# Kernel tuning notes

Hardware: AMD Instinct MI355X
Metric: run time of the kernel (lower is better)

## Reference

```python
import jax, jax.numpy as jnp
import numpy as np

NH, NKV, HD = 16, 8, 128  # heads, kv heads, head dim
N_REP = NH // NKV
EPS = 1e-06
K_MASK = float(jnp.finfo(jnp.bfloat16).min)
SCALE = HD ** -0.5


def _rms_norm(x, w):
    xf = x.astype(jnp.float32)
    rms = jnp.sqrt(jnp.mean(xf * xf, axis=-1, keepdims=True) + EPS)
    return (xf / rms * w).astype(x.dtype)


def _rotate_half(x):
    x1, x2 = jnp.split(x, 2, axis=-1)
    return jnp.concatenate([-x2, x1], axis=-1)


def setup_inputs() -> dict:
    key = jax.random.key(0)
    ks = jax.random.split(key, 5)
    B, S, H = 1, 2048, 2048
    hidden_states = jax.random.normal(ks[0], (B, S, H), jnp.float32)
    # real RoPE tables (duplicated-half layout), theta = 5e6
    pos = jnp.arange(S, dtype=jnp.float32)
    inv_freq = 1.0 / (5_000_000.0 ** (jnp.arange(0, HD, 2, dtype=jnp.float32) / HD))
    ang = pos[:, None] * inv_freq[None, :]            # (S, HD/2)
    emb = jnp.concatenate([ang, ang], axis=-1)[None]  # (1, S, HD)
    cos, sin = jnp.cos(emb), jnp.sin(emb)
    attention_mask = jnp.tril(jnp.ones((S, S), bool))[None, None]  # causal (1,1,S,S)
    sc = 0.02
    wq = jax.random.normal(ks[1], (H, NH * HD), jnp.float32) * sc
    wk = jax.random.normal(ks[2], (H, NKV * HD), jnp.float32) * sc
    wv = jax.random.normal(ks[3], (H, NKV * HD), jnp.float32) * sc
    wo = jax.random.normal(ks[4], (NH * HD, H), jnp.float32) * sc
    q_norm_w = jnp.ones((HD,), jnp.float32)
    k_norm_w = jnp.ones((HD,), jnp.float32)
    return {"hidden_states": hidden_states, "cos": cos, "sin": sin,
            "attention_mask": attention_mask, "wq": wq, "wk": wk, "wv": wv,
            "wo": wo, "q_norm_w": q_norm_w, "k_norm_w": k_norm_w}


def reference(hidden_states, cos, sin, attention_mask, wq, wk, wv, wo, q_norm_w, k_norm_w):
    B, S, H = hidden_states.shape
    q = (hidden_states @ wq).reshape(B, S, NH, HD)
    k = (hidden_states @ wk).reshape(B, S, NKV, HD)
    v = (hidden_states @ wv).reshape(B, S, NKV, HD)
    q = _rms_norm(q, q_norm_w)
    k = _rms_norm(k, k_norm_w)
    c = cos[:, :, None, :]
    s = sin[:, :, None, :]
    q = q * c + _rotate_half(q) * s
    k = k * c + _rotate_half(k) * s
    # GQA: group q heads by kv head; same math as jnp.repeat + matmul
    qg = q.reshape(B, S, NKV, N_REP, HD)
    scores = jnp.einsum('bqgrd,bkgd->bgrqk', qg, k) * SCALE  # (B,NKV,N_REP,S,S)
    scores = jnp.where(attention_mask[:, :, None], scores, K_MASK)
    attn = jax.nn.softmax(scores.astype(jnp.float32), axis=-1).astype(q.dtype)
    out = jnp.einsum('bgrqk,bkgd->bqgrd', attn, v)            # (B,S,NKV,N_REP,HD)
    out = out.reshape(B, S, NH * HD)
    return out @ wo
```

## Files before the change

kernel.cpp:

```cpp
#include <hip/hip_runtime.h>
#include <hip/hip_bf16.h>
#include <stdint.h>

typedef _Float16 half8 __attribute__((ext_vector_type(8)));
typedef _Float16 half4 __attribute__((ext_vector_type(4)));
typedef float f32x4 __attribute__((ext_vector_type(4)));

#define MFMA16(A, B, C) __builtin_amdgcn_mfma_f32_16x16x32_f16(A, B, C, 0, 0, 0)

static constexpr int Sdim = 2048;
static constexpr int NH = 16;
static constexpr int NKV = 8;
static constexpr int HD = 128;
static constexpr float ATT_SCALE = 0.08838834764831845f;
static constexpr float S0 = 4.0f;

__device__ __forceinline__ void async_copy16(const _Float16* g, _Float16* l) {
  auto gp = reinterpret_cast<const __attribute__((address_space(1))) uint32_t*>(
      reinterpret_cast<uintptr_t>(g));
  auto lp = reinterpret_cast<__attribute__((address_space(3))) uint32_t*>(
      reinterpret_cast<uintptr_t>(l));
  __builtin_amdgcn_global_load_lds(gp, lp, 16, 0, 0);
}

__global__ __launch_bounds__(256) void xconv(const float* __restrict__ X,
                                             _Float16* __restrict__ Xh) {
  int i = (blockIdx.x * 256 + threadIdx.x) * 4;
  float4 v = *(const float4*)(X + i);
  half4 h = {(_Float16)v.x, (_Float16)v.y, (_Float16)v.z, (_Float16)v.w};
  *(half4*)(Xh + i) = h;
}

__global__ __launch_bounds__(256) void wtrans_all(const float* __restrict__ wq,
                                                  const float* __restrict__ wk,
                                                  const float* __restrict__ wv,
                                                  const float* __restrict__ wo,
                                                  _Float16* __restrict__ wqT,
                                                  _Float16* __restrict__ wkT,
                                                  _Float16* __restrict__ wvT,
                                                  _Float16* __restrict__ woT) {
  const float* W;
  _Float16* WT;
  int N;
  switch (blockIdx.z) {
    case 0: W = wq; WT = wqT; N = 2048; break;
    case 1: W = wk; WT = wkT; N = 1024; break;
    case 2: W = wv; WT = wvT; N = 1024; break;
    default: W = wo; WT = woT; N = 2048; break;
  }
  if ((int)blockIdx.x * 64 >= N) return;
  const int K = 2048;
  __shared__ __align__(16) float tile[64][68];
  int n0 = blockIdx.x * 64, k0 = blockIdx.y * 64;
  int t = threadIdx.x;
  int c = (t & 15) * 4;
  int rb = t >> 4;
  for (int p = 0; p < 4; ++p) {
    int k = p * 16 + rb;
    *(float4*)&tile[k][c] = *(const float4*)(W + (size_t)(k0 + k) * N + n0 + c);
  }
  __syncthreads();
  int n = t >> 2;
  int kc = (t & 3) * 16;
  half8 o0, o1;
  for (int i = 0; i < 8; ++i) {
    o0[i] = (_Float16)tile[kc + i][n];
    o1[i] = (_Float16)tile[kc + 8 + i][n];
  }
  _Float16* dst = WT + (size_t)(n0 + n) * K + k0 + kc;
  *(half8*)dst = o0;
  *(half8*)(dst + 8) = o1;
}

template <int NI>
__device__ __forceinline__ void stage64(const _Float16* __restrict__ src, size_t stride,
                                        int k0, _Float16* lds, int w, int lane) {
  for (int ii = 0; ii < NI; ++ii) {
    int i = w * NI + ii;
    int row = i * 8 + (lane >> 3);
    int c = (lane & 7) ^ (row & 7);
    async_copy16(src + (size_t)row * stride + k0 + c * 8, lds + i * 512);
  }
}

__device__ __forceinline__ int frag_off(int row, int ks, int quad, int col) {
  return row * 64 + (((ks << 2) | quad) ^ (col & 7)) * 8;
}

__global__ __launch_bounds__(256, 2) void gemm_qkv(const _Float16* __restrict__ Xh,
                                                   const _Float16* __restrict__ wqT,
                                                   const _Float16* __restrict__ wkT,
                                                   const _Float16* __restrict__ wvT,
                                                   const float* __restrict__ cs,
                                                   const float* __restrict__ sn,
                                                   const float* __restrict__ qw,
                                                   const float* __restrict__ kw,
                                                   _Float16* __restrict__ Qn,
                                                   _Float16* __restrict__ Kn,
                                                   _Float16* __restrict__ Vt) {
  __shared__ __align__(16) _Float16 SH[4 * 128 * 64];
  int bx = blockIdx.x, m0 = blockIdx.y * 128;
  const _Float16* BT;
  _Float16* outp;
  int n0, Nst;
  bool vt;
  if (bx < 16)      { BT = wqT; outp = Qn; n0 = bx * 128;        vt = false; Nst = 2048; }
  else if (bx < 24) { BT = wkT; outp = Kn; n0 = (bx - 16) * 128; vt = false; Nst = 1024; }
  else              { BT = wvT; outp = Vt; n0 = (bx - 24) * 128; vt = true;  Nst = 2048; }
  int t = threadIdx.x, lane = t & 63, w = t >> 6;
  int col = lane & 15, quad = lane >> 4;
  int wm = (w & 1) * 64, wn = (w >> 1) * 64;
  const _Float16* Ap = Xh + (size_t)m0 * 2048;
  const _Float16* Bp = BT + (size_t)n0 * 2048;
  f32x4 acc[4][4] = {};
  stage64<4>(Ap, 2048, 0, SH, w, lane);
  stage64<4>(Bp, 2048, 0, SH + 16384, w, lane);
#pragma unroll 1
  for (int it = 0; it < 32; ++it) {
    int c = it & 1;
    if (it + 1 < 32) {
      stage64<4>(Ap, 2048, (it + 1) * 64, SH + (c ^ 1) * 8192, w, lane);
      stage64<4>(Bp, 2048, (it + 1) * 64, SH + 16384 + (c ^ 1) * 8192, w, lane);
      asm volatile("s_waitcnt vmcnt(8)" ::: "memory");
    } else {
      asm volatile("s_waitcnt vmcnt(0)" ::: "memory");
    }
    __builtin_amdgcn_sched_barrier(0);
    __builtin_amdgcn_s_barrier();
    __builtin_amdgcn_sched_barrier(0);
    const _Float16* Asc = SH + c * 8192;
    const _Float16* Bsc = SH + 16384 + c * 8192;
    half8 af[4][2], bf[4][2];
    for (int i = 0; i < 4; ++i)
      for (int ks = 0; ks < 2; ++ks) {
        af[i][ks] = *(const half8*)(Asc + frag_off(wm + i * 16 + col, ks, quad, col));
        bf[i][ks] = *(const half8*)(Bsc + frag_off(wn + i * 16 + col, ks, quad, col));
      }
    __builtin_amdgcn_s_setprio(1);
    if (!vt) {
      for (int ks = 0; ks < 2; ++ks)
        for (int i = 0; i < 4; ++i)
          for (int j = 0; j < 4; ++j)
            acc[i][j] = MFMA16(bf[j][ks], af[i][ks], acc[i][j]);
    } else {
      for (int ks = 0; ks < 2; ++ks)
        for (int i = 0; i < 4; ++i)
          for (int j = 0; j < 4; ++j)
            acc[i][j] = MFMA16(af[i][ks], bf[j][ks], acc[i][j]);
    }
    __builtin_amdgcn_s_setprio(0);
    __builtin_amdgcn_sched_barrier(0);
    __builtin_amdgcn_s_barrier();
    __builtin_amdgcn_sched_barrier(0);
  }
  if (!vt) {
    __syncthreads();
    for (int i = 0; i < 4; ++i)
      for (int j = 0; j < 4; ++j) {
        int m = wm + i * 16 + col;
        int d = wn + j * 16 + quad * 4;
        half4 hv = {(_Float16)acc[i][j][0], (_Float16)acc[i][j][1],
                    (_Float16)acc[i][j][2], (_Float16)acc[i][j][3]};
        *(half4*)(SH + m * 132 + d) = hv;
      }
    __syncthreads();
    const float* nw = (bx < 16) ? qw : kw;
    float scale = (bx < 16) ? ATT_SCALE : 1.0f;
    float w0 = nw[lane], w1 = nw[lane + 64];
#pragma unroll 1
    for (int it2 = 0; it2 < 32; it2 += 4) {
      float x0[4], x1[4], c0[4], c1[4], sv0[4], sv1[4];
#pragma unroll
      for (int u = 0; u < 4; ++u) {
        int row = w * 32 + it2 + u;
        int m = m0 + row;
        c0[u] = cs[m * HD + lane];
        c1[u] = cs[m * HD + lane + 64];
        sv0[u] = sn[m * HD + lane];
        sv1[u] = sn[m * HD + lane + 64];
        x0[u] = (float)SH[row * 132 + lane];
        x1[u] = (float)SH[row * 132 + 64 + lane];
      }
#pragma unroll
      for (int u = 0; u < 4; ++u) {
        float ss = x0[u] * x0[u] + x1[u] * x1[u];
#pragma unroll
        for (int o = 32; o > 0; o >>= 1) ss += __shfl_xor(ss, o);
        float inv = rsqrtf(ss * (1.0f / 128.0f) + 1e-6f);
        float n0v = x0[u] * inv * w0, n1v = x1[u] * inv * w1;
        int m = m0 + w * 32 + it2 + u;
        _Float16* q = outp + (size_t)m * Nst + n0;
        q[lane] = (_Float16)((n0v * c0[u] - n1v * sv0[u]) * scale);
        q[lane + 64] = (_Float16)((n1v * c1[u] + n0v * sv1[u]) * scale);
      }
    }
  } else {
    for (int i = 0; i < 4; ++i)
      for (int j = 0; j < 4; ++j) {
        int n = n0 + wn + j * 16 + col;
        int mb = m0 + wm + i * 16 + quad * 4;
        half4 hv = {(_Float16)acc[i][j][0], (_Float16)acc[i][j][1],
                    (_Float16)acc[i][j][2], (_Float16)acc[i][j][3]};
        *(half4*)(outp + (size_t)n * Sdim + mb) = hv;
      }
  }
}

__global__ __launch_bounds__(256, 2) void gemm_o(const _Float16* __restrict__ A,
                                                 const _Float16* __restrict__ BT,
                                                 float* __restrict__ C) {
  __shared__ __align__(16) _Float16 As[2][64 * 64];
  __shared__ __align__(16) _Float16 Bs[2][128 * 64];
  int m0 = blockIdx.y * 64, n0 = blockIdx.x * 128;
  int t = threadIdx.x, lane = t & 63, w = t >> 6;
  int col = lane & 15, quad = lane >> 4;
  int wm = (w & 1) * 32, wn = (w >> 1) * 64;
  const _Float16* Ap = A + (size_t)m0 * 2048;
  const _Float16* Bp = BT + (size_t)n0 * 2048;
  f32x4 acc[2][4] = {};
  stage64<2>(Ap, 2048, 0, As[0], w, lane);
  stage64<4>(Bp, 2048, 0, Bs[0], w, lane);
#pragma unroll 1
  for (int it = 0; it < 32; ++it) {
    int c = it & 1;
    if (it + 1 < 32) {
      stage64<2>(Ap, 2048, (it + 1) * 64, As[c ^ 1], w, lane);
      stage64<4>(Bp, 2048, (it + 1) * 64, Bs[c ^ 1], w, lane);
      asm volatile("s_waitcnt vmcnt(6)" ::: "memory");
    } else {
      asm volatile("s_waitcnt vmcnt(0)" ::: "memory");
    }
    __builtin_amdgcn_sched_barrier(0);
    __builtin_amdgcn_s_barrier();
    __builtin_amdgcn_sched_barrier(0);
    half8 af[2][2], bf[4][2];
    for (int ks = 0; ks < 2; ++ks) {
      for (int i = 0; i < 2; ++i)
        af[i][ks] = *(const half8*)(As[c] + frag_off(wm + i * 16 + col, ks, quad, col));
      for (int j = 0; j < 4; ++j)
        bf[j][ks] = *(const half8*)(Bs[c] + frag_off(wn + j * 16 + col, ks, quad, col));
    }
    __builtin_amdgcn_s_setprio(1);
    for (int ks = 0; ks < 2; ++ks)
      for (int i = 0; i < 2; ++i)
        for (int j = 0; j < 4; ++j)
          acc[i][j] = MFMA16(bf[j][ks], af[i][ks], acc[i][j]);
    __builtin_amdgcn_s_setprio(0);
    __builtin_amdgcn_sched_barrier(0);
    __builtin_amdgcn_s_barrier();
    __builtin_amdgcn_sched_barrier(0);
  }
  for (int i = 0; i < 2; ++i)
    for (int j = 0; j < 4; ++j) {
      int m = m0 + wm + i * 16 + col;
      int n = n0 + wn + j * 16 + quad * 4;
      *(f32x4*)(C + (size_t)m * 2048 + n) = acc[i][j];
    }
}

__device__ __forceinline__ void attn_tile(const half8* qf, f32x4* O, float& li,
                                          const _Float16* Ksb, const _Float16* Vsb,
                                          _Float16* Psw, bool domask,
                                          int col, int quad, int w) {
  f32x4 Sc[4];
  __builtin_amdgcn_s_setprio(1);
  for (int nt = 0; nt < 4; ++nt) {
    f32x4 a = {};
    for (int kc = 0; kc < 4; ++kc) {
      half8 b = *(const half8*)(Ksb + (nt * 16 + col) * 128 + ((4 * kc + quad) ^ col) * 8);
      a = MFMA16(b, qf[kc], a);
    }
    Sc[nt] = a;
  }
  __builtin_amdgcn_s_setprio(0);
  if (domask) {
    for (int nt = 0; nt < 4; ++nt)
      for (int r = 0; r < 4; ++r)
        if ((nt * 16 + quad * 4 + r) > (w * 16 + col)) Sc[nt][r] = -1e4f;
  }
  for (int nt = 0; nt < 4; ++nt) {
    half4 pk;
    for (int r = 0; r < 4; ++r) {
      float pv = __expf(Sc[nt][r] - S0);
      li += pv;
      pk[r] = (_Float16)pv;
    }
    *(half4*)(Psw + col * 64 + (((2 * nt + (quad >> 1)) ^ (col & 7)) << 3) +
              ((quad & 1) << 2)) = pk;
  }
  __builtin_amdgcn_s_setprio(1);
  for (int c2 = 0; c2 < 2; ++c2) {
    half8 ap = *(const half8*)(Psw + col * 64 + (((4 * c2 + quad) ^ (col & 7)) * 8));
    for (int nt = 0; nt < 8; ++nt) {
      half8 bv = *(const half8*)(Vsb + (nt * 16 + col) * 64 +
                                 (((4 * c2 + quad) ^ (col & 7)) * 8));
      O[nt] = MFMA16(ap, bv, O[nt]);
    }
  }
  __builtin_amdgcn_s_setprio(0);
}

__global__ __launch_bounds__(256, 2) void fattn(const _Float16* __restrict__ Qn,
                                                const _Float16* __restrict__ Kn,
                                                const _Float16* __restrict__ Vt,
                                                _Float16* __restrict__ Op01,
                                                float* __restrict__ lp) {
  __shared__ __align__(16) _Float16 Ks[2][64 * 128];
  __shared__ __align__(16) _Float16 Vs[2][128 * 64];
  __shared__ __align__(16) _Float16 Ps[4 * 1024];
  int f = blockIdx.x;
  int Wk = (f & 7) * 64 + (f >> 3);
  int xb = Wk & 15, h = (Wk >> 4) & 15, s = Wk >> 8;
  int g = h >> 1;
  int qb0 = 31 - xb, qb1 = xb;
  int t = threadIdx.x, lane = t & 63, w = t >> 6;
  int col = lane & 15, quad = lane >> 4;
  _Float16* Psw = Ps + w * 1024;
  _Float16* op = Op01 + (size_t)s * Sdim * (NH * HD);
  float* lpp = lp + (size_t)s * NH * Sdim + (size_t)h * Sdim;

  auto stageKV = [&](int b, int kt) {
    for (int ii = 0; ii < 4; ++ii) {
      int i = w * 4 + ii;
      int krow = i * 4 + (lane >> 4);
      int kc = (lane & 15) ^ (krow & 15);
      async_copy16(Kn + (size_t)(kt * 64 + krow) * (NKV * HD) + g * HD + kc * 8,
                   Ks[b] + i * 512);
      int vrow = i * 8 + (lane >> 3);
      int vc = (lane & 7) ^ (vrow & 7);
      async_copy16(Vt + (size_t)(g * HD + vrow) * Sdim + kt * 64 + vc * 8,
                   Vs[b] + i * 512);
    }
  };

  half8 qf0[4], qf1[4];
  {
    int qr0 = qb0 * 64 + w * 16 + col;
    int qr1 = qb1 * 64 + w * 16 + col;
    for (int kc = 0; kc < 4; ++kc) {
      qf0[kc] = *(const half8*)(Qn + (size_t)qr0 * (NH * HD) + h * HD + kc * 32 + quad * 8);
      qf1[kc] = *(const half8*)(Qn + (size_t)qr1 * (NH * HD) + h * HD + kc * 32 + quad * 8);
    }
  }
  f32x4 O0[8] = {}, O1[8] = {};
  float li0 = 0.0f, li1 = 0.0f;

  int nt = (qb0 - s) / 2 + 1;
  stageKV(0, s);
#pragma unroll 1
  for (int it = 0; it < nt; ++it) {
    int kt = s + it * 2;
    int c = it & 1;
    if (it + 1 < nt) {
      stageKV(c ^ 1, kt + 2);
      asm volatile("s_waitcnt vmcnt(8)" ::: "memory");
    } else {
      asm volatile("s_waitcnt vmcnt(0)" ::: "memory");
    }
    __builtin_amdgcn_sched_barrier(0);
    __builtin_amdgcn_s_barrier();
    __builtin_amdgcn_sched_barrier(0);
    const _Float16* Kb = Ks[c];
    const _Float16* Vb = Vs[c];
    if (kt <= qb1) {
      attn_tile(qf0, O0, li0, Kb, Vb, Psw, false, col, quad, w);
      attn_tile(qf1, O1, li1, Kb, Vb, Psw, kt == qb1, col, quad, w);
    } else {
      attn_tile(qf0, O0, li0, Kb, Vb, Psw, kt == qb0, col, quad, w);
    }
    __builtin_amdgcn_sched_barrier(0);
    __builtin_amdgcn_s_barrier();
    __builtin_amdgcn_sched_barrier(0);
  }

  auto finish = [&](f32x4* O, float li, int qb) {
    li += __shfl_xor(li, 16);
    li += __shfl_xor(li, 32);
    for (int ntile = 0; ntile < 8; ++ntile)
      for (int r = 0; r < 4; ++r) {
        int m = qb * 64 + w * 16 + quad * 4 + r;
        op[(size_t)m * (NH * HD) + h * HD + ntile * 16 + col] = (_Float16)O[ntile][r];
      }
    if (quad == 0) lpp[qb * 64 + w * 16 + col] = li;
  };
  finish(O0, li0, qb0);
  finish(O1, li1, qb1);
}

__global__ __launch_bounds__(256) void merge(const _Float16* __restrict__ Op01,
                                             const float* __restrict__ lp,
                                             _Float16* __restrict__ attn) {
  int m = blockIdx.x, t = threadIdx.x;
  int h = t >> 4, d0 = (t & 15) * 8;
  size_t off = (size_t)m * (NH * HD) + h * HD + d0;
  half8 o0 = *(const half8*)(Op01 + off);
  half8 o1 = *(const half8*)(Op01 + (size_t)Sdim * NH * HD + off);
  float l = lp[(size_t)h * Sdim + m] +
            lp[(size_t)NH * Sdim + (size_t)h * Sdim + m];
  float ri = 1.0f / l;
  half8 o;
  for (int i = 0; i < 8; ++i)
    o[i] = (_Float16)(((float)o0[i] + (float)o1[i]) * ri);
  *(half8*)(attn + off) = o;
}

extern "C" void kernel_launch(void* const* d_in, const int* in_sizes, int n_in,
                              void* d_out, int out_size, void* d_ws, size_t ws_size,
                              hipStream_t stream) {
  (void)in_sizes; (void)n_in; (void)out_size; (void)ws_size;
  const float* X  = (const float*)d_in[0];
  const float* cs = (const float*)d_in[1];
  const float* sn = (const float*)d_in[2];
  const float* wq = (const float*)d_in[4];
  const float* wk = (const float*)d_in[5];
  const float* wv = (const float*)d_in[6];
  const float* wo = (const float*)d_in[7];
  const float* qw = (const float*)d_in[8];
  const float* kw = (const float*)d_in[9];
  char* ws = (char*)d_ws;
  const size_t MB = 1024 * 1024;
  _Float16* wqT  = (_Float16*)(ws + 0 * MB);
  _Float16* wkT  = (_Float16*)(ws + 8 * MB);
  _Float16* wvT  = (_Float16*)(ws + 12 * MB);
  _Float16* woT  = (_Float16*)(ws + 16 * MB);
  _Float16* Xh   = (_Float16*)(ws + 24 * MB);
  _Float16* attn = (_Float16*)(ws + 32 * MB);
  _Float16* Vt   = (_Float16*)(ws + 44 * MB);
  _Float16* Qn   = (_Float16*)(ws + 48 * MB);
  _Float16* Kn   = (_Float16*)(ws + 56 * MB);
  float*    lp   = (float*)(ws + 60 * MB);
  _Float16* Op01 = wqT;
  float* out = (float*)d_out;

  xconv<<<4096, 256, 0, stream>>>(X, Xh);
  wtrans_all<<<dim3(32, 32, 4), 256, 0, stream>>>(wq, wk, wv, wo, wqT, wkT, wvT, woT);

  gemm_qkv<<<dim3(32, 16), 256, 0, stream>>>(Xh, wqT, wkT, wvT, cs, sn, qw, kw,
                                             Qn, Kn, Vt);

  fattn<<<512, 256, 0, stream>>>(Qn, Kn, Vt, Op01, lp);
  merge<<<2048, 256, 0, stream>>>(Op01, lp, attn);

  gemm_o<<<dim3(16, 32), 256, 0, stream>>>(attn, woT, out);
}
```

Before: 237.3 us.

## Read V operands directly from global memory instead of staging in LDS

Removes the double-buffered V tile from shared memory and has each wave load its V fragments for the PV MFMA straight from global memory (L2/L1) in two batches of four. This cuts LDS footprint and async-copy traffic and relaxes the vmcnt wait. In exchange, every wave reloads V from global memory with long latency inside the compute loop, and the loads are shared by no other waves in the block, adding redundant global traffic. The async-copy wait counting may also be disturbed by the new plain global loads.

```diff
diff --git a/kernel.cpp b/kernel.cpp
--- a/kernel.cpp
+++ b/kernel.cpp
@@ -259,7 +259,7 @@
 }
 
 __device__ __forceinline__ void attn_tile(const half8* qf, f32x4* O, float& li,
-                                          const _Float16* Ksb, const _Float16* Vsb,
+                                          const _Float16* Ksb, const _Float16* Vg,
                                           _Float16* Psw, bool domask,
                                           int col, int quad, int w) {
   f32x4 Sc[4];
@@ -291,11 +291,19 @@
   __builtin_amdgcn_s_setprio(1);
   for (int c2 = 0; c2 < 2; ++c2) {
     half8 ap = *(const half8*)(Psw + col * 64 + (((4 * c2 + quad) ^ (col & 7)) * 8));
-    for (int nt = 0; nt < 8; ++nt) {
-      half8 bv = *(const half8*)(Vsb + (nt * 16 + col) * 64 +
-                                 (((4 * c2 + quad) ^ (col & 7)) * 8));
-      O[nt] = MFMA16(ap, bv, O[nt]);
-    }
+    half8 bv[4];
+#pragma unroll
+    for (int nt = 0; nt < 4; ++nt)
+      bv[nt] = *(const half8*)(Vg + (size_t)(nt * 16 + col) * Sdim + (4 * c2 + quad) * 8);
+#pragma unroll
+    for (int nt = 0; nt < 4; ++nt) O[nt] = MFMA16(ap, bv[nt], O[nt]);
+    half8 bv2[4];
+#pragma unroll
+    for (int nt = 0; nt < 4; ++nt)
+      bv2[nt] = *(const half8*)(Vg + (size_t)((nt + 4) * 16 + col) * Sdim +
+                                (4 * c2 + quad) * 8);
+#pragma unroll
+    for (int nt = 0; nt < 4; ++nt) O[nt + 4] = MFMA16(ap, bv2[nt], O[nt + 4]);
   }
   __builtin_amdgcn_s_setprio(0);
 }
@@ -306,7 +314,6 @@
                                                 _Float16* __restrict__ Op01,
                                                 float* __restrict__ lp) {
   __shared__ __align__(16) _Float16 Ks[2][64 * 128];
-  __shared__ __align__(16) _Float16 Vs[2][128 * 64];
   __shared__ __align__(16) _Float16 Ps[4 * 1024];
   int f = blockIdx.x;
   int Wk = (f & 7) * 64 + (f >> 3);
@@ -318,18 +325,15 @@
   _Float16* Psw = Ps + w * 1024;
   _Float16* op = Op01 + (size_t)s * Sdim * (NH * HD);
   float* lpp = lp + (size_t)s * NH * Sdim + (size_t)h * Sdim;
-
-  auto stageKV = [&](int b, int kt) {
+  const _Float16* Vbase = Vt + (size_t)g * HD * Sdim;
+
+  auto stageK = [&](int b, int kt) {
     for (int ii = 0; ii < 4; ++ii) {
       int i = w * 4 + ii;
       int krow = i * 4 + (lane >> 4);
       int kc = (lane & 15) ^ (krow & 15);
       async_copy16(Kn + (size_t)(kt * 64 + krow) * (NKV * HD) + g * HD + kc * 8,
                    Ks[b] + i * 512);
-      int vrow = i * 8 + (lane >> 3);
-      int vc = (lane & 7) ^ (vrow & 7);
-      async_copy16(Vt + (size_t)(g * HD + vrow) * Sdim + kt * 64 + vc * 8,
-                   Vs[b] + i * 512);
     }
   };
 
@@ -346,14 +350,14 @@
   float li0 = 0.0f, li1 = 0.0f;
 
   int nt = (qb0 - s) / 2 + 1;
-  stageKV(0, s);
+  stageK(0, s);
 #pragma unroll 1
   for (int it = 0; it < nt; ++it) {
     int kt = s + it * 2;
     int c = it & 1;
     if (it + 1 < nt) {
-      stageKV(c ^ 1, kt + 2);
-      asm volatile("s_waitcnt vmcnt(8)" ::: "memory");
+      stageK(c ^ 1, kt + 2);
+      asm volatile("s_waitcnt vmcnt(4)" ::: "memory");
     } else {
       asm volatile("s_waitcnt vmcnt(0)" ::: "memory");
     }
@@ -361,12 +365,12 @@
     __builtin_amdgcn_s_barrier();
     __builtin_amdgcn_sched_barrier(0);
     const _Float16* Kb = Ks[c];
-    const _Float16* Vb = Vs[c];
+    const _Float16* Vg = Vbase + kt * 64;
     if (kt <= qb1) {
-      attn_tile(qf0, O0, li0, Kb, Vb, Psw, false, col, quad, w);
-      attn_tile(qf1, O1, li1, Kb, Vb, Psw, kt == qb1, col, quad, w);
+      attn_tile(qf0, O0, li0, Kb, Vg, Psw, false, col, quad, w);
+      attn_tile(qf1, O1, li1, Kb, Vg, Psw, kt == qb1, col, quad, w);
     } else {
-      attn_tile(qf0, O0, li0, Kb, Vb, Psw, kt == qb0, col, quad, w);
+      attn_tile(qf0, O0, li0, Kb, Vg, Psw, kt == qb0, col, quad, w);
     }
     __builtin_amdgcn_sched_barrier(0);
     __builtin_amdgcn_s_barrier();
```

After: 301.6 us. 27.1% more time.
